# Optimization experiments

Measured on AMD Instinct MI355X. Metric: run time of the kernel, lower is better.

Reference implementation:

```python
import jax, jax.numpy as jnp
import numpy as np

D_MODEL = 1024
N_HEADS = 16
D_HEAD = D_MODEL // N_HEADS
LATENT = 32
NEG = -1e9


def setup_inputs() -> dict:
    key = jax.random.key(0)
    ks = jax.random.split(key, 6)
    B, T = 2, 4096
    x = jax.random.normal(ks[0], (B, T, D_MODEL), dtype=jnp.float32)
    s = lambda fan_in: 1.0 / np.sqrt(fan_in)
    W_kv = jax.random.normal(ks[1], (D_MODEL, LATENT), dtype=jnp.float32) * s(D_MODEL)
    W_k = jax.random.normal(ks[2], (LATENT, D_MODEL), dtype=jnp.float32) * s(LATENT)
    W_v = jax.random.normal(ks[3], (LATENT, D_MODEL), dtype=jnp.float32) * s(LATENT)
    W_q = jax.random.normal(ks[4], (D_MODEL, D_MODEL), dtype=jnp.float32) * s(D_MODEL)
    W_o = jax.random.normal(ks[5], (D_MODEL, D_MODEL), dtype=jnp.float32) * s(D_MODEL)
    return {"x": x, "W_kv": W_kv, "W_k": W_k, "W_v": W_v, "W_q": W_q, "W_o": W_o}


def reference(x, W_kv, W_k, W_v, W_q, W_o):
    B, T, _ = x.shape
    # low-rank latent compression of KV path
    lat = jnp.einsum('btd,dl->btl', x, W_kv)              # [B,T,latent]
    def sp(t):  # [B,T,D] -> [B,H,T,dh]
        return t.reshape(B, T, N_HEADS, D_HEAD).transpose(0, 2, 1, 3)
    K = sp(jnp.einsum('btl,ld->btd', lat, W_k))
    V = sp(jnp.einsum('btl,ld->btd', lat, W_v))
    Q = sp(jnp.einsum('btd,de->bte', x, W_q))
    scale = 1.0 / jnp.sqrt(jnp.float32(D_HEAD))
    s = jnp.einsum('bhqd,bhkd->bhqk', Q, K) * scale       # [B,H,T,T]
    causal = jnp.tril(jnp.ones((T, T), dtype=jnp.float32))
    s = s + (1.0 - causal) * NEG
    attn = jax.nn.softmax(s, axis=-1)
    out = jnp.einsum('bhqk,bhkd->bhqd', attn, V)          # [B,H,T,dh]
    out = out.transpose(0, 2, 1, 3).reshape(B, T, D_MODEL)
    return jnp.einsum('btd,de->bte', out, W_o)
```

## Files before the change

kernel.cpp:

```cpp
#include <hip/hip_runtime.h>
#include <hip/hip_bf16.h>


#define T_SEQ  4096
#define NHEAD  16
#define DHEAD  64
#define DMODEL 1024
#define LATENT 32
#define BATCH  2
#define M_ROWS (BATCH * T_SEQ)

typedef __attribute__((ext_vector_type(8))) short bf16x8;
typedef __attribute__((ext_vector_type(4))) float f32x4;

__device__ __forceinline__ short f2bf(float f) {
  __hip_bfloat16 h = __float2bfloat16(f);
  return __builtin_bit_cast(short, h);
}

__device__ __forceinline__ float exp2_hw(float x) {
  return __builtin_amdgcn_exp2f(x);
}

__device__ __forceinline__ void gld_lds16(const short* g, short* l) {
  __builtin_amdgcn_global_load_lds(
      (const __attribute__((address_space(1))) void*)g,
      (__attribute__((address_space(3))) void*)l, 16, 0, 0);
}

__global__ __launch_bounds__(256)
void convert_in(const float* __restrict__ src, short* __restrict__ dst, int n) {
  int i = (blockIdx.x * 256 + threadIdx.x) * 4;
  if (i >= n) return;
  const f32x4 v = *(const f32x4*)(src + i);
  short4 o;
  o.x = f2bf(v[0]); o.y = f2bf(v[1]); o.z = f2bf(v[2]); o.w = f2bf(v[3]);
  *(short4*)(dst + i) = o;
}

__global__ __launch_bounds__(256)
void prep_weights(const float* __restrict__ Wq, const float* __restrict__ Wk,
                  const float* __restrict__ Wv, const float* __restrict__ Wo,
                  const float* __restrict__ Wkv,
                  short* __restrict__ WcombT, short* __restrict__ WvoT) {
  const int blk = blockIdx.x;
  const int tid = threadIdx.x;

  if (blk < 64) {
    __shared__ float wk[32 * 64];
    const int h   = blk >> 2;
    const int dm0 = (blk & 3) * 256;
    {
      const int l  = tid >> 3;
      const int d0 = (tid & 7) * 8;
      *(f32x4*)(wk + l * 64 + d0)     = *(const f32x4*)(Wk + (size_t)l * DMODEL + h * 64 + d0);
      *(f32x4*)(wk + l * 64 + d0 + 4) = *(const f32x4*)(Wk + (size_t)l * DMODEL + h * 64 + d0 + 4);
    }
    __syncthreads();
    const int dm = dm0 + tid;
    float acc[32] = {};
    for (int dv = 0; dv < 16; ++dv) {
      const f32x4 wq = *(const f32x4*)(Wq + (size_t)dm * DMODEL + h * 64 + dv * 4);
#pragma unroll
      for (int jj = 0; jj < 4; ++jj)
#pragma unroll
        for (int l = 0; l < 32; ++l)
          acc[l] += wq[jj] * wk[l * 64 + dv * 4 + jj];
    }
    const float SCALE = 0.1803368801111f;
#pragma unroll
    for (int l = 0; l < 32; ++l)
      WcombT[((size_t)(h * 32 + l)) * DMODEL + dm] = f2bf(acc[l] * SCALE);
  } else if (blk < 128) {
    __shared__ float wvs[32 * 64];
    const int h  = (blk - 64) >> 2;
    const int n0 = ((blk - 64) & 3) * 256;
    {
      const int l  = tid >> 3;
      const int d0 = (tid & 7) * 8;
      *(f32x4*)(wvs + l * 64 + d0)     = *(const f32x4*)(Wv + (size_t)l * DMODEL + h * 64 + d0);
      *(f32x4*)(wvs + l * 64 + d0 + 4) = *(const f32x4*)(Wv + (size_t)l * DMODEL + h * 64 + d0 + 4);
    }
    __syncthreads();
    const int n = n0 + tid;
    float acc[32] = {};
    for (int d = 0; d < 64; ++d) {
      const float wo = Wo[(size_t)(h * 64 + d) * DMODEL + n];
#pragma unroll
      for (int l = 0; l < 32; ++l)
        acc[l] += wvs[l * 64 + d] * wo;
    }
#pragma unroll
    for (int l = 0; l < 32; ++l)
      WvoT[(size_t)n * 512 + h * 32 + l] = f2bf(acc[l]);
  } else {
    const int i = (blk - 128) * 256 + tid;
    const int k = i >> 5;
    const int l = i & 31;
    WcombT[(size_t)(512 + l) * DMODEL + k] = f2bf(Wkv[(size_t)k * LATENT + l]);
    short* z = WcombT + (size_t)544 * DMODEL + (size_t)i * 3;
    z[0] = 0; z[1] = 0; z[2] = 0;
  }
}

__global__ __launch_bounds__(256)
void gemm128_kernel(const short* __restrict__ A, const short* __restrict__ Bt,
                    short* __restrict__ Cs, float* __restrict__ Cf,
                    short* __restrict__ Cs2, short* __restrict__ Cs3,
                    int M, int K, int N, int out_mode) {
  __shared__ short Alds[128 * 32];
  __shared__ short Blds[128 * 32];

  const int tid  = threadIdx.x;
  const int wv   = tid >> 6;
  const int lane = tid & 63;
  const int quad = lane >> 4;
  const int l16  = lane & 15;
  const int wm   = wv >> 1;
  const int wn   = wv & 1;

  const int nb  = N >> 7;
  const int nwg = gridDim.x;
  int bid = blockIdx.x;
  if ((nwg & 7) == 0)
    bid = (bid & 7) * (nwg >> 3) + (bid >> 3);
  const int mt = bid / nb;
  const int nt = bid - mt * nb;
  const int m0 = mt << 7;
  const int n0 = nt << 7;

  const int rl  = lane >> 2;
  const int cl  = lane & 3;
  const int csw = cl ^ ((rl >> 1) & 3);
  const int ra  = wv * 16 + rl;
  const short* Ag0 = A  + (size_t)(m0 + ra) * K + csw * 8;
  const short* Ag1 = A  + (size_t)(m0 + 64 + ra) * K + csw * 8;
  const short* Bg0 = Bt + (size_t)(n0 + ra) * K + csw * 8;
  const short* Bg1 = Bt + (size_t)(n0 + 64 + ra) * K + csw * 8;
  short* Al0 = &Alds[(wv * 16) * 32];
  short* Al1 = &Alds[(64 + wv * 16) * 32];
  short* Bl0 = &Blds[(wv * 16) * 32];
  short* Bl1 = &Blds[(64 + wv * 16) * 32];

  const int rsw = (l16 >> 1) & 3;
  const int coff = (quad ^ rsw) * 8;

  f32x4 acc[4][4] = {};

  for (int k0 = 0; k0 < K; k0 += 32) {
    gld_lds16(Ag0 + k0, Al0);
    gld_lds16(Ag1 + k0, Al1);
    gld_lds16(Bg0 + k0, Bl0);
    gld_lds16(Bg1 + k0, Bl1);
    __builtin_amdgcn_s_waitcnt(0x0F70);
    __syncthreads();

    bf16x8 af[4], bfr[4];
#pragma unroll
    for (int i = 0; i < 4; ++i) {
      const int rowA = wm * 64 + i * 16 + l16;
      const int rowB = wn * 64 + i * 16 + l16;
      af[i]  = *(const bf16x8*)&Alds[rowA * 32 + coff];
      bfr[i] = *(const bf16x8*)&Blds[rowB * 32 + coff];
    }
#pragma unroll
    for (int i = 0; i < 4; ++i)
#pragma unroll
      for (int j = 0; j < 4; ++j)
        acc[i][j] = __builtin_amdgcn_mfma_f32_16x16x32_bf16(af[i], bfr[j], acc[i][j], 0, 0, 0);
    __syncthreads();
  }

#pragma unroll
  for (int i = 0; i < 4; ++i) {
    const int row = m0 + wm * 64 + i * 16 + quad * 4;
#pragma unroll
    for (int j = 0; j < 4; ++j) {
      const int col = n0 + wn * 64 + j * 16 + l16;
#pragma unroll
      for (int r = 0; r < 4; ++r) {
        if (out_mode == 3) {
          Cf[(size_t)(row + r) * N + col] = acc[i][j][r];
        } else {
          if (col < 512) {
            Cs[(size_t)(row + r) * 512 + col] = f2bf(acc[i][j][r]);
          } else if (col < 544) {
            const short v = f2bf(acc[i][j][r]);
            const int l = col - 512;
            const int m = row + r;
            Cs2[(size_t)m * LATENT + l] = v;
            const int bb = m >> 12;
            const int tt = m & (T_SEQ - 1);
            Cs3[((size_t)(bb * LATENT + l) << 12) + tt] = v;
          }
        }
      }
    }
  }
}

__global__ __launch_bounds__(256, 4)
void attn_kernel(const short* __restrict__ Qlat, short* __restrict__ Olat,
                 const short* __restrict__ latg, const short* __restrict__ latTg) {
  __shared__ short Klds[64 * 32];
  __shared__ short Vlds[32 * 64];
  __shared__ short Plds[4][2][16 * 72];

  const int tid  = threadIdx.x;
  const int wv   = tid >> 6;
  const int lane = tid & 63;
  const int quad = lane >> 4;
  const int l16  = lane & 15;

  const int idx = blockIdx.x;
  const int xcd = idx & 7;
  const int j   = idx >> 3;
  const int bhg = xcd * 2 + (j & 1);
  const int jj  = j >> 1;
  const int a   = jj >> 4;
  const int r_  = jj & 15;
  const int qb  = (a & 1) ? ((a == 1 ? 0 : 16) + r_) : ((a == 0 ? 63 : 47) - r_);
  const int b   = bhg >> 3;
  const int hg  = bhg & 7;

  const int q0 = qb * 64;
  const int qw = q0 + wv * 16;
  const int q  = qw + l16;

  const int srK = wv * 16 + (lane >> 2);
  const int scK = (lane & 3) ^ ((srK >> 1) & 3);
  const short* Ksrc = latg + ((size_t)b * T_SEQ + srK) * LATENT + scK * 8;
  const int srV = wv * 8 + (lane >> 3);
  const int scV = (lane & 7) ^ (srV & 7);
  const short* Vsrc = latTg + ((size_t)b * LATENT + srV) * T_SEQ + scV * 8;

  const short* Qrow = Qlat + ((size_t)(b * T_SEQ) + qw + l16) * 512 + hg * 64;
  const bf16x8 qfA = *(const bf16x8*)(Qrow + quad * 8);
  const bf16x8 qfB = *(const bf16x8*)(Qrow + 32 + quad * 8);

  bf16x8 ones;
#pragma unroll
  for (int i = 0; i < 8; ++i) ones[i] = (short)0x3F80;

  f32x4 oA[2] = {}, oB[2] = {};
  f32x4 laccA = {}, laccB = {};
  short* PA = &Plds[wv][0][0];
  short* PB = &Plds[wv][1][0];

  auto kv_step = [&](const int k0, const bool diag) {
    gld_lds16(Ksrc + (size_t)k0 * LATENT, &Klds[(wv * 16) * 32]);
    gld_lds16(Vsrc + k0,                  &Vlds[(wv * 8) * 64]);
    __builtin_amdgcn_s_waitcnt(0x0F70);
    __syncthreads();

    f32x4 sa[4], sb[4];
    __builtin_amdgcn_s_setprio(1);
#pragma unroll
    for (int mt = 0; mt < 4; ++mt) {
      if (diag && mt > wv) {
        sa[mt][0] = sa[mt][1] = sa[mt][2] = sa[mt][3] = -1e9f;
        sb[mt] = sa[mt];
        continue;
      }
      const int R = mt * 16 + l16;
      const bf16x8 kf = *(const bf16x8*)&Klds[R * 32 + ((quad ^ ((R >> 1) & 3))) * 8];
      f32x4 z = {};
      sa[mt] = __builtin_amdgcn_mfma_f32_16x16x32_bf16(kf, qfA, z, 0, 0, 0);
      sb[mt] = __builtin_amdgcn_mfma_f32_16x16x32_bf16(kf, qfB, z, 0, 0, 0);
    }
    __builtin_amdgcn_s_setprio(0);

    if (diag) {
#pragma unroll
      for (int mt = 0; mt < 4; ++mt)
#pragma unroll
        for (int r = 0; r < 4; ++r) {
          const int key = k0 + mt * 16 + quad * 4 + r;
          if (key > q) { sa[mt][r] = -1e9f; sb[mt][r] = -1e9f; }
        }
    }

#pragma unroll
    for (int mt = 0; mt < 4; ++mt)
#pragma unroll
      for (int r = 0; r < 4; ++r) {
        sa[mt][r] = exp2_hw(sa[mt][r]);
        sb[mt][r] = exp2_hw(sb[mt][r]);
      }

    asm volatile("" ::: "memory");
#pragma unroll
    for (int mt = 0; mt < 4; ++mt) {
      short4 wA, wB;
      wA.x = f2bf(sa[mt][0]); wA.y = f2bf(sa[mt][1]);
      wA.z = f2bf(sa[mt][2]); wA.w = f2bf(sa[mt][3]);
      *(short4*)(PA + l16 * 72 + mt * 16 + quad * 4) = wA;
      wB.x = f2bf(sb[mt][0]); wB.y = f2bf(sb[mt][1]);
      wB.z = f2bf(sb[mt][2]); wB.w = f2bf(sb[mt][3]);
      *(short4*)(PB + l16 * 72 + mt * 16 + quad * 4) = wB;
    }
    asm volatile("" ::: "memory");
    __builtin_amdgcn_s_waitcnt(0xC07F);
    asm volatile("" ::: "memory");
    const bf16x8 pfA0 = *(const bf16x8*)(PA + l16 * 72 + quad * 8);
    const bf16x8 pfA1 = *(const bf16x8*)(PA + l16 * 72 + 32 + quad * 8);
    const bf16x8 pfB0 = *(const bf16x8*)(PB + l16 * 72 + quad * 8);
    const bf16x8 pfB1 = *(const bf16x8*)(PB + l16 * 72 + 32 + quad * 8);
    asm volatile("" ::: "memory");

    __builtin_amdgcn_s_setprio(1);
#pragma unroll
    for (int f = 0; f < 2; ++f) {
      const int R = f * 16 + l16;
      const bf16x8 vf0 = *(const bf16x8*)&Vlds[R * 64 + ((quad    ) ^ (R & 7)) * 8];
      const bf16x8 vf1 = *(const bf16x8*)&Vlds[R * 64 + ((quad + 4) ^ (R & 7)) * 8];
      oA[f] = __builtin_amdgcn_mfma_f32_16x16x32_bf16(vf0, pfA0, oA[f], 0, 0, 0);
      oA[f] = __builtin_amdgcn_mfma_f32_16x16x32_bf16(vf1, pfA1, oA[f], 0, 0, 0);
      oB[f] = __builtin_amdgcn_mfma_f32_16x16x32_bf16(vf0, pfB0, oB[f], 0, 0, 0);
      oB[f] = __builtin_amdgcn_mfma_f32_16x16x32_bf16(vf1, pfB1, oB[f], 0, 0, 0);
    }
    laccA = __builtin_amdgcn_mfma_f32_16x16x32_bf16(ones, pfA0, laccA, 0, 0, 0);
    laccA = __builtin_amdgcn_mfma_f32_16x16x32_bf16(ones, pfA1, laccA, 0, 0, 0);
    laccB = __builtin_amdgcn_mfma_f32_16x16x32_bf16(ones, pfB0, laccB, 0, 0, 0);
    laccB = __builtin_amdgcn_mfma_f32_16x16x32_bf16(ones, pfB1, laccB, 0, 0, 0);
    __builtin_amdgcn_s_setprio(0);
    __syncthreads();
  };

#pragma unroll 1
  for (int k0 = 0; k0 < q0; k0 += 64) kv_step(k0, false);
  kv_step(q0, true);

  const float invA = 1.0f / laccA[0];
  const float invB = 1.0f / laccB[0];
  short* Orow = Olat + ((size_t)(b * T_SEQ) + qw + l16) * 512 + hg * 64;
#pragma unroll
  for (int f = 0; f < 2; ++f) {
    short4 wA, wB;
    wA.x = f2bf(oA[f][0] * invA); wA.y = f2bf(oA[f][1] * invA);
    wA.z = f2bf(oA[f][2] * invA); wA.w = f2bf(oA[f][3] * invA);
    *(short4*)(Orow + f * 16 + quad * 4) = wA;
    wB.x = f2bf(oB[f][0] * invB); wB.y = f2bf(oB[f][1] * invB);
    wB.z = f2bf(oB[f][2] * invB); wB.w = f2bf(oB[f][3] * invB);
    *(short4*)(Orow + 32 + f * 16 + quad * 4) = wB;
  }
}

extern "C" void kernel_launch(void* const* d_in, const int* in_sizes, int n_in,
                              void* d_out, int out_size, void* d_ws, size_t ws_size,
                              hipStream_t stream) {
  const float* x   = (const float*)d_in[0];
  const float* Wkv = (const float*)d_in[1];
  const float* Wk  = (const float*)d_in[2];
  const float* Wv  = (const float*)d_in[3];
  const float* Wq  = (const float*)d_in[4];
  const float* Wo  = (const float*)d_in[5];

  char* p = (char*)d_ws;
  auto carve = [&](size_t n) {
    char* r = p;
    p += (n + 255) & ~(size_t)255;
    return r;
  };
  short* xbf    = (short*)carve((size_t)M_ROWS * DMODEL * 2);
  short* Qlat   = (short*)carve((size_t)M_ROWS * 512 * 2);
  short* Olat   = (short*)carve((size_t)M_ROWS * 512 * 2);
  short* lat    = (short*)carve((size_t)M_ROWS * LATENT * 2);
  short* latT   = (short*)carve((size_t)M_ROWS * LATENT * 2);
  short* WcombT = (short*)carve((size_t)640 * DMODEL * 2);
  short* WvoT   = (short*)carve((size_t)DMODEL * 512 * 2);

  convert_in<<<(M_ROWS * DMODEL / 4 + 255) / 256, 256, 0, stream>>>(x, xbf, M_ROWS * DMODEL);
  prep_weights<<<256, 256, 0, stream>>>(Wq, Wk, Wv, Wo, Wkv, WcombT, WvoT);

  gemm128_kernel<<<(M_ROWS / 128) * (640 / 128), 256, 0, stream>>>(
      xbf, WcombT, Qlat, nullptr, lat, latT, M_ROWS, DMODEL, 640, 5);

  attn_kernel<<<1024, 256, 0, stream>>>(Qlat, Olat, lat, latT);

  gemm128_kernel<<<(M_ROWS / 128) * (DMODEL / 128), 256, 0, stream>>>(
      Olat, WvoT, nullptr, (float*)d_out, nullptr, nullptr, M_ROWS, 512, DMODEL, 3);
}
```

Measured before the change: 146.4 us.

## Split causal attention KV range across two blocks and add combine kernel

Each query block's causal KV range is split into two halves, handled by separate workgroups, doubling the attention grid. The work order becomes longest-first. Each half writes unnormalized fp32 partial outputs and row sums to workspace, and a new combine kernel adds the two halves, normalizes and converts to bf16. The goal is shorter per-block critical paths and better load balance. The cost is extra global traffic for the fp32 partials, an additional kernel launch, and the loss of the previous paired-block balancing scheme.

Measured after the change: 149.0 us. Within noise of the previous version (+1.8%).

```diff
diff --git a/kernel.cpp b/kernel.cpp
--- a/kernel.cpp
+++ b/kernel.cpp
@@ -200,7 +200,8 @@
 }
 
 __global__ __launch_bounds__(256, 4)
-void attn_kernel(const short* __restrict__ Qlat, short* __restrict__ Olat,
+void attn_kernel(const short* __restrict__ Qlat, float* __restrict__ Opart,
+                 float* __restrict__ lpart,
                  const short* __restrict__ latg, const short* __restrict__ latTg) {
   __shared__ short Klds[64 * 32];
   __shared__ short Vlds[32 * 64];
@@ -216,16 +217,20 @@
   const int xcd = idx & 7;
   const int j   = idx >> 3;
   const int bhg = xcd * 2 + (j & 1);
-  const int jj  = j >> 1;
-  const int a   = jj >> 4;
-  const int r_  = jj & 15;
-  const int qb  = (a & 1) ? ((a == 1 ? 0 : 16) + r_) : ((a == 0 ? 63 : 47) - r_);
+  const int rest = j >> 1;
+  const int half = rest >> 6;
+  const int qb   = 63 - (rest & 63);
   const int b   = bhg >> 3;
   const int hg  = bhg & 7;
 
   const int q0 = qb * 64;
   const int qw = q0 + wv * 16;
   const int q  = qw + l16;
+
+  const int ntt  = qb + 1;
+  const int n0h  = (ntt + 1) >> 1;
+  const int tbeg = half ? n0h : 0;
+  const int tend = half ? ntt : n0h;
 
   const int srK = wv * 16 + (lane >> 2);
   const int scK = (lane & 3) ^ ((srK >> 1) & 3);
@@ -328,22 +333,51 @@
   };
 
 #pragma unroll 1
-  for (int k0 = 0; k0 < q0; k0 += 64) kv_step(k0, false);
-  kv_step(q0, true);
-
-  const float invA = 1.0f / laccA[0];
-  const float invB = 1.0f / laccB[0];
-  short* Orow = Olat + ((size_t)(b * T_SEQ) + qw + l16) * 512 + hg * 64;
+  for (int t = tbeg; t < tend; ++t)
+    kv_step(t * 64, t == qb);
+
+  float* Obase = Opart + (size_t)half * M_ROWS * 512 +
+                 ((size_t)(b * T_SEQ) + qw + l16) * 512 + hg * 64;
 #pragma unroll
   for (int f = 0; f < 2; ++f) {
-    short4 wA, wB;
-    wA.x = f2bf(oA[f][0] * invA); wA.y = f2bf(oA[f][1] * invA);
-    wA.z = f2bf(oA[f][2] * invA); wA.w = f2bf(oA[f][3] * invA);
-    *(short4*)(Orow + f * 16 + quad * 4) = wA;
-    wB.x = f2bf(oB[f][0] * invB); wB.y = f2bf(oB[f][1] * invB);
-    wB.z = f2bf(oB[f][2] * invB); wB.w = f2bf(oB[f][3] * invB);
-    *(short4*)(Orow + 32 + f * 16 + quad * 4) = wB;
+    *(f32x4*)(Obase + f * 16 + quad * 4)      = oA[f];
+    *(f32x4*)(Obase + 32 + f * 16 + quad * 4) = oB[f];
   }
+  if (quad == 0) {
+    float* lrow = lpart + (size_t)half * M_ROWS * NHEAD +
+                  ((size_t)(b * T_SEQ) + qw + l16) * NHEAD + hg * 2;
+    lrow[0] = laccA[0];
+    lrow[1] = laccB[0];
+  }
+}
+
+__global__ __launch_bounds__(256)
+void combine_kernel(const float* __restrict__ Opart,
+                    const float* __restrict__ lpart,
+                    short* __restrict__ Olat) {
+  const int idx = blockIdx.x * 256 + threadIdx.x;
+  const int m = idx >> 6;
+  const int g = idx & 63;
+  const int h = g >> 2;
+
+  const float* p0 = Opart + (size_t)m * 512 + g * 8;
+  const float* p1 = p0 + (size_t)M_ROWS * 512;
+  const float l = lpart[(size_t)m * NHEAD + h] +
+                  lpart[(size_t)M_ROWS * NHEAD + (size_t)m * NHEAD + h];
+  const float inv = 1.0f / l;
+
+  const f32x4 a0 = *(const f32x4*)p0;
+  const f32x4 a1 = *(const f32x4*)(p0 + 4);
+  const f32x4 b0 = *(const f32x4*)p1;
+  const f32x4 b1 = *(const f32x4*)(p1 + 4);
+
+  short4 w0, w1;
+  w0.x = f2bf((a0[0] + b0[0]) * inv); w0.y = f2bf((a0[1] + b0[1]) * inv);
+  w0.z = f2bf((a0[2] + b0[2]) * inv); w0.w = f2bf((a0[3] + b0[3]) * inv);
+  w1.x = f2bf((a1[0] + b1[0]) * inv); w1.y = f2bf((a1[1] + b1[1]) * inv);
+  w1.z = f2bf((a1[2] + b1[2]) * inv); w1.w = f2bf((a1[3] + b1[3]) * inv);
+  *(short4*)(Olat + (size_t)m * 512 + g * 8)     = w0;
+  *(short4*)(Olat + (size_t)m * 512 + g * 8 + 4) = w1;
 }
 
 extern "C" void kernel_launch(void* const* d_in, const int* in_sizes, int n_in,
@@ -369,6 +403,8 @@
   short* latT   = (short*)carve((size_t)M_ROWS * LATENT * 2);
   short* WcombT = (short*)carve((size_t)640 * DMODEL * 2);
   short* WvoT   = (short*)carve((size_t)DMODEL * 512 * 2);
+  float* Opart  = (float*)carve((size_t)2 * M_ROWS * 512 * 4);
+  float* lpart  = (float*)carve((size_t)2 * M_ROWS * NHEAD * 4);
 
   convert_in<<<(M_ROWS * DMODEL / 4 + 255) / 256, 256, 0, stream>>>(x, xbf, M_ROWS * DMODEL);
   prep_weights<<<256, 256, 0, stream>>>(Wq, Wk, Wv, Wo, Wkv, WcombT, WvoT);
@@ -376,7 +412,8 @@
   gemm128_kernel<<<(M_ROWS / 128) * (640 / 128), 256, 0, stream>>>(
       xbf, WcombT, Qlat, nullptr, lat, latT, M_ROWS, DMODEL, 640, 5);
 
-  attn_kernel<<<1024, 256, 0, stream>>>(Qlat, Olat, lat, latT);
+  attn_kernel<<<2048, 256, 0, stream>>>(Qlat, Opart, lpart, lat, latT);
+  combine_kernel<<<M_ROWS * 64 / 256, 256, 0, stream>>>(Opart, lpart, Olat);
 
   gemm128_kernel<<<(M_ROWS / 128) * (DMODEL / 128), 256, 0, stream>>>(
       Olat, WvoT, nullptr, (float*)d_out, nullptr, nullptr, M_ROWS, 512, DMODEL, 3);
```
